# Kernel tuning notes

Hardware: AMD Instinct MI355X
Metric: run time of the kernel (lower is better)

The kernel has to match this reference:

```python
import jax, jax.numpy as jnp
import numpy as np

N_NODES = 65536
N_EDGES = 1048576
IN_FEATS = 128
N_HIDDEN = 64
N_LAYERS = 2
EPS = 1e-12  # matches torch F.normalize default eps


def setup_inputs() -> dict:
    key = jax.random.key(0)
    ks = jax.random.split(key, 8)
    features = jax.random.normal(ks[0], (N_NODES, IN_FEATS), dtype=jnp.float32)
    src = jax.random.randint(ks[1], (N_EDGES,), 0, N_NODES)
    dst = jax.random.randint(ks[2], (N_EDGES,), 0, N_NODES)
    W1 = jax.random.normal(ks[3], (IN_FEATS, N_HIDDEN), dtype=jnp.float32) * (1.0 / np.sqrt(IN_FEATS))
    b1 = jax.random.normal(ks[4], (N_HIDDEN,), dtype=jnp.float32) * 0.01
    W2 = jax.random.normal(ks[5], (N_HIDDEN, N_HIDDEN), dtype=jnp.float32) * (1.0 / np.sqrt(N_HIDDEN))
    b2 = jax.random.normal(ks[6], (N_HIDDEN,), dtype=jnp.float32) * 0.01
    betas = jnp.ones((N_LAYERS,), dtype=jnp.float32)  # init_beta=1, learnable
    return {"features": features, "src": src, "dst": dst,
            "W1": W1, "b1": b1, "W2": W2, "b2": b2, "betas": betas}


def agnn_conv(h, src, dst, beta, n_nodes):
    # L2-normalize node features (F.normalize, p=2)
    norm = jnp.sqrt(jnp.sum(h * h, axis=-1, keepdims=True))
    nh = h / jnp.maximum(norm, EPS)
    # cosine similarity along each edge: e_ij = beta * <nh_src, nh_dst>
    cos = jnp.sum(nh[src] * nh[dst], axis=-1)          # [E]
    e = beta * cos
    # edge softmax over incoming edges of each dst node (numerically stable)
    m = jax.ops.segment_max(e, dst, num_segments=n_nodes)   # [N], -inf for 0-in-degree
    ex = jnp.exp(e - m[dst])                                 # [E]
    s = jax.ops.segment_sum(ex, dst, num_segments=n_nodes)   # [N]
    alpha = ex / s[dst]                                      # [E]
    # weighted aggregation of UN-normalized source features
    out = jax.ops.segment_sum(alpha[:, None] * h[src], dst, num_segments=n_nodes)
    return out


def reference(features, src, dst, W1, b1, W2, b2, betas):
    h = jax.nn.relu(features @ W1 + b1)        # proj: Linear + ReLU
    for i in range(N_LAYERS):                   # stacked AGNNConv layers
        h = agnn_conv(h, src, dst, betas[i], N_NODES)
    return h @ W2 + b2                          # cls: Linear
```

## Files before the change

### kernel.cpp

```cpp
#include <hip/hip_runtime.h>

#define N_NODES 65536
#define N_EDGES 1048576
#define IN_FEATS 128
#define N_HIDDEN 64

static constexpr float F_EPS = 1e-12f;

template <int K, bool RELU, bool RN>
__device__ __forceinline__ void gemm_body(const float* __restrict__ A,
                                          const float* __restrict__ W,
                                          const float* __restrict__ bias,
                                          float* __restrict__ C,
                                          float* __restrict__ rn,
                                          int block64, int tid, float* Wl) {
  int lane = tid & 63;
  int wave = tid >> 6;
  float bv = bias[lane];
  int r0 = block64 * 64 + wave * 16;

  float a[16][K / 64];
#pragma unroll
  for (int r = 0; r < 16; ++r)
#pragma unroll
    for (int c = 0; c < K / 64; ++c)
      a[r][c] = A[(size_t)(r0 + r) * K + c * 64 + lane];

  float acc[16];
#pragma unroll
  for (int r = 0; r < 16; ++r) acc[r] = bv;

  const float4* W4 = reinterpret_cast<const float4*>(W);
  float4* Wl4 = reinterpret_cast<float4*>(Wl);

#pragma unroll
  for (int c = 0; c < K / 64; ++c) {
    __syncthreads();
#pragma unroll
    for (int i = tid; i < 64 * 16; i += 256) Wl4[i] = W4[c * 64 * 16 + i];
    __syncthreads();
#pragma unroll 8
    for (int kk = 0; kk < 64; ++kk) {
      float w = Wl[kk * 64 + lane];
#pragma unroll
      for (int r = 0; r < 16; ++r) {
        float av = __uint_as_float(
            __builtin_amdgcn_readlane(__float_as_uint(a[r][c]), kk));
        acc[r] = fmaf(av, w, acc[r]);
      }
    }
  }

#pragma unroll
  for (int r = 0; r < 16; ++r) {
    float v = acc[r];
    if (RELU) v = fmaxf(v, 0.0f);
    C[(size_t)(r0 + r) * 64 + lane] = v;
    if (RN) {
      float ss = v * v;
#pragma unroll
      for (int off = 32; off > 0; off >>= 1) ss += __shfl_xor(ss, off, 64);
      if (lane == 0) rn[r0 + r] = 1.0f / fmaxf(sqrtf(ss), F_EPS);
    }
  }
}

__global__ __launch_bounds__(256) void proj_scatter_k(
    const float* __restrict__ A, const float* __restrict__ W,
    const float* __restrict__ bias, float* __restrict__ C, float* __restrict__ rn,
    const int* __restrict__ src, const int* __restrict__ dst,
    int* __restrict__ deg2, int* __restrict__ csr) {
  __shared__ float Wl[64 * 64];
  int bb = blockIdx.x;
  int g = bb / 5;
  int r = bb % 5;
  if (r == 4) {
    gemm_body<IN_FEATS, true, true>(A, W, bias, C, rn, g, threadIdx.x, Wl);
  } else {
    int t = (g * 4 + r) * 256 + threadIdx.x;
    int d = dst[t];
    int s = src[t];
    int rep = t & 1;
    int p = atomicAdd(&deg2[rep * N_NODES + d], 1);
    if (p < 32) csr[(d << 6) + (rep << 5) + p] = s;
  }
}

template <int K, bool RELU, bool RN>
__global__ __launch_bounds__(256) void gemm64_k(const float* __restrict__ A,
                                                const float* __restrict__ W,
                                                const float* __restrict__ bias,
                                                float* __restrict__ C,
                                                float* __restrict__ rn) {
  __shared__ float Wl[64 * 64];
  gemm_body<K, RELU, RN>(A, W, bias, C, rn, blockIdx.x, threadIdx.x, Wl);
}

__global__ __launch_bounds__(256) void agnn_k(const float* __restrict__ X,
                                              const float* __restrict__ rn,
                                              const int* __restrict__ deg2,
                                              const int* __restrict__ csr,
                                              const float* __restrict__ betas, int layer,
                                              float* __restrict__ Y,
                                              float* __restrict__ rn_out) {
  int node = blockIdx.x * 4 + (threadIdx.x >> 6);
  int lane = threadIdx.x & 63;
  int sl = lane & 3;
  int g = lane >> 2;
  float beta = betas[layer];

  const float4* X4 = reinterpret_cast<const float4*>(X);
  float4 hd[4];
#pragma unroll
  for (int q = 0; q < 4; ++q) hd[q] = X4[(size_t)node * 16 + sl + 4 * q];
  float rnd = rn[node] * beta;

  int d0 = deg2[node];
  int d1 = deg2[N_NODES + node];
  d0 = d0 > 32 ? 32 : d0;
  d1 = d1 > 32 ? 32 : d1;
  int d = d0 + d1;
  int base = node << 6;

  float ssum = 0.0f;
  float4 acc[4];
#pragma unroll
  for (int q = 0; q < 4; ++q) acc[q] = make_float4(0.f, 0.f, 0.f, 0.f);

  bool act0 = (g < d);
  int slot0 = (g < d0) ? g : (g - d0 + 32);
  int s0 = act0 ? csr[base + slot0] : node;
  float4 hs0[4];
#pragma unroll
  for (int q = 0; q < 4; ++q) hs0[q] = X4[(size_t)s0 * 16 + sl + 4 * q];
  float rs0 = rn[s0];

  for (int i = 0; i < d; i += 16) {
    int j1 = i + 16 + g;
    bool act1 = (j1 < d);
    int slot1 = (j1 < d0) ? j1 : (j1 - d0 + 32);
    int s1 = act1 ? csr[base + slot1] : node;
    float4 hs1[4];
#pragma unroll
    for (int q = 0; q < 4; ++q) hs1[q] = X4[(size_t)s1 * 16 + sl + 4 * q];
    float rs1 = rn[s1];

    float pa = hd[0].x * hs0[0].x;
    pa = fmaf(hd[0].y, hs0[0].y, pa);
    pa = fmaf(hd[0].z, hs0[0].z, pa);
    pa = fmaf(hd[0].w, hs0[0].w, pa);
    pa = fmaf(hd[1].x, hs0[1].x, pa);
    pa = fmaf(hd[1].y, hs0[1].y, pa);
    pa = fmaf(hd[1].z, hs0[1].z, pa);
    pa = fmaf(hd[1].w, hs0[1].w, pa);
    float pb = hd[2].x * hs0[2].x;
    pb = fmaf(hd[2].y, hs0[2].y, pb);
    pb = fmaf(hd[2].z, hs0[2].z, pb);
    pb = fmaf(hd[2].w, hs0[2].w, pb);
    pb = fmaf(hd[3].x, hs0[3].x, pb);
    pb = fmaf(hd[3].y, hs0[3].y, pb);
    pb = fmaf(hd[3].z, hs0[3].z, pb);
    pb = fmaf(hd[3].w, hs0[3].w, pb);
    float p = pa + pb;
    p += __shfl_xor(p, 1, 64);
    p += __shfl_xor(p, 2, 64);
    float ex = act0 ? __expf(p * rnd * rs0) : 0.0f;
    ssum += ex;
#pragma unroll
    for (int q = 0; q < 4; ++q) {
      acc[q].x = fmaf(ex, hs0[q].x, acc[q].x);
      acc[q].y = fmaf(ex, hs0[q].y, acc[q].y);
      acc[q].z = fmaf(ex, hs0[q].z, acc[q].z);
      acc[q].w = fmaf(ex, hs0[q].w, acc[q].w);
    }

#pragma unroll
    for (int q = 0; q < 4; ++q) hs0[q] = hs1[q];
    rs0 = rs1;
    act0 = act1;
  }

#pragma unroll
  for (int off = 4; off < 64; off <<= 1) {
    ssum += __shfl_xor(ssum, off, 64);
#pragma unroll
    for (int q = 0; q < 4; ++q) {
      acc[q].x += __shfl_xor(acc[q].x, off, 64);
      acc[q].y += __shfl_xor(acc[q].y, off, 64);
      acc[q].z += __shfl_xor(acc[q].z, off, 64);
      acc[q].w += __shfl_xor(acc[q].w, off, 64);
    }
  }

  float inv = (ssum > 0.0f) ? (1.0f / ssum) : 0.0f;
#pragma unroll
  for (int q = 0; q < 4; ++q) {
    acc[q].x *= inv; acc[q].y *= inv; acc[q].z *= inv; acc[q].w *= inv;
  }

  if (g == 0) {
    float4* Y4 = reinterpret_cast<float4*>(Y);
#pragma unroll
    for (int q = 0; q < 4; ++q) Y4[(size_t)node * 16 + sl + 4 * q] = acc[q];
  }

  float ss = 0.0f;
#pragma unroll
  for (int q = 0; q < 4; ++q)
    ss += acc[q].x * acc[q].x + acc[q].y * acc[q].y +
          acc[q].z * acc[q].z + acc[q].w * acc[q].w;
  ss += __shfl_xor(ss, 1, 64);
  ss += __shfl_xor(ss, 2, 64);
  if (lane == 0) rn_out[node] = 1.0f / fmaxf(sqrtf(ss), F_EPS);
}

extern "C" void kernel_launch(void* const* d_in, const int* in_sizes, int n_in,
                              void* d_out, int out_size, void* d_ws, size_t ws_size,
                              hipStream_t stream) {
  const float* features = (const float*)d_in[0];
  const int* src = (const int*)d_in[1];
  const int* dst = (const int*)d_in[2];
  const float* W1 = (const float*)d_in[3];
  const float* b1 = (const float*)d_in[4];
  const float* W2 = (const float*)d_in[5];
  const float* b2 = (const float*)d_in[6];
  const float* betas = (const float*)d_in[7];
  float* out = (float*)d_out;

  char* ws = (char*)d_ws;
  size_t off = 0;
  auto alloc = [&](size_t bytes) {
    void* p = ws + off;
    off += (bytes + 255) & ~255UL;
    return p;
  };
  float* hA = (float*)alloc((size_t)N_NODES * 64 * 4);
  float* hB = (float*)alloc((size_t)N_NODES * 64 * 4);
  float* rnA = (float*)alloc((size_t)N_NODES * 4);
  float* rnB = (float*)alloc((size_t)N_NODES * 4);
  int* deg2 = (int*)alloc((size_t)2 * N_NODES * 4);
  int* csr = (int*)alloc((size_t)N_NODES * 64 * 4);

  hipMemsetAsync(deg2, 0, (size_t)2 * N_NODES * 4, stream);

  proj_scatter_k<<<5120, 256, 0, stream>>>(features, W1, b1, hA, rnA,
                                           src, dst, deg2, csr);

  agnn_k<<<N_NODES / 4, 256, 0, stream>>>(hA, rnA, deg2, csr, betas, 0, hB, rnB);

  agnn_k<<<N_NODES / 4, 256, 0, stream>>>(hB, rnB, deg2, csr, betas, 1, hA, rnA);

  gemm64_k<N_HIDDEN, false, false><<<N_NODES / 64, 256, 0, stream>>>(hA, W2, b2, out, nullptr);
}
```

Before: 312.0 us.

## Build CSR via two-pass bucketed scatter with shared-memory atomics

Replaces the single global-atomic scatter into a split two-replica CSR with a two-pass build. The first pass buckets edges by destination range in shared memory and flushes them in chunks to global buckets. The second pass, fused with the projection GEMM, places each bucket's edges into a contiguous per-node CSR using shared-memory atomics. This removes heavy global atomic contention and the replica slot arithmetic in the aggregation kernel, at the cost of an extra kernel launch and an intermediate buffer round trip. Fixed bucket capacities (BCAP, and a per-node cap of 64) can silently drop edges on skewed inputs.

Measured after the change: 391.2 us. 25.4% more time.

```diff
diff --git a/kernel.cpp b/kernel.cpp
--- a/kernel.cpp
+++ b/kernel.cpp
@@ -4,8 +4,51 @@
 #define N_EDGES 1048576
 #define IN_FEATS 128
 #define N_HIDDEN 64
+#define NBUCK 128
+#define BCAP 10240
+#define LCAP 40
 
 static constexpr float F_EPS = 1e-12f;
+
+__global__ __launch_bounds__(256) void passA_bucket_k(const int* __restrict__ src,
+                                                      const int* __restrict__ dst,
+                                                      int* __restrict__ gcnt,
+                                                      int2* __restrict__ gbuf) {
+  __shared__ int lcnt[NBUCK];
+  __shared__ int2 lbuf[NBUCK][LCAP];
+  int tid = threadIdx.x;
+  int b = blockIdx.x;
+  if (tid < NBUCK) lcnt[tid] = 0;
+  __syncthreads();
+
+  for (int i = b * 4096 + tid; i < (b + 1) * 4096; i += 256) {
+    int d = dst[i];
+    int s = src[i];
+    int k = d >> 9;
+    int p = atomicAdd(&lcnt[k], 1);
+    if (p < LCAP) {
+      lbuf[k][p] = make_int2(s, d);
+    } else {
+      int gp = atomicAdd(&gcnt[k], 1);
+      gbuf[(size_t)k * BCAP + gp] = make_int2(s, d);
+    }
+  }
+  __syncthreads();
+
+  int lane = tid & 63;
+  int w = tid >> 6;
+  for (int kk = 0; kk < 32; ++kk) {
+    int k = w * 32 + kk;
+    int L = lcnt[k];
+    L = L < LCAP ? L : LCAP;
+    if (L == 0) continue;
+    int pos;
+    if (lane == 0) pos = atomicAdd(&gcnt[k], L);
+    pos = __shfl(pos, 0, 64);
+    for (int j = lane; j < L; j += 64)
+      gbuf[(size_t)k * BCAP + pos + j] = lbuf[k][j];
+  }
+}
 
 template <int K, bool RELU, bool RN>
 __device__ __forceinline__ void gemm_body(const float* __restrict__ A,
@@ -65,24 +108,35 @@
   }
 }
 
-__global__ __launch_bounds__(256) void proj_scatter_k(
+__global__ __launch_bounds__(256) void place_proj_k(
     const float* __restrict__ A, const float* __restrict__ W,
     const float* __restrict__ bias, float* __restrict__ C, float* __restrict__ rn,
-    const int* __restrict__ src, const int* __restrict__ dst,
-    int* __restrict__ deg2, int* __restrict__ csr) {
+    const int* __restrict__ gcnt, const int2* __restrict__ gbuf,
+    int* __restrict__ deg, int* __restrict__ csr) {
   __shared__ float Wl[64 * 64];
   int bb = blockIdx.x;
-  int g = bb / 5;
-  int r = bb % 5;
-  if (r == 4) {
-    gemm_body<IN_FEATS, true, true>(A, W, bias, C, rn, g, threadIdx.x, Wl);
+  int g = bb / 9;
+  int r = bb % 9;
+  if (r == 8) {
+    int tid = threadIdx.x;
+    int* lcnt = (int*)Wl;
+    for (int j = tid; j < 512; j += 256) lcnt[j] = 0;
+    __syncthreads();
+    int E = gcnt[g];
+    E = E < BCAP ? E : BCAP;
+    for (int i = tid; i < E; i += 256) {
+      int2 e = gbuf[(size_t)g * BCAP + i];
+      int nn = e.y & 511;
+      int rk = atomicAdd(&lcnt[nn], 1);
+      if (rk < 64) csr[((size_t)e.y << 6) + rk] = e.x;
+    }
+    __syncthreads();
+    for (int j = tid; j < 512; j += 256) {
+      int dv = lcnt[j];
+      deg[g * 512 + j] = dv < 64 ? dv : 64;
+    }
   } else {
-    int t = (g * 4 + r) * 256 + threadIdx.x;
-    int d = dst[t];
-    int s = src[t];
-    int rep = t & 1;
-    int p = atomicAdd(&deg2[rep * N_NODES + d], 1);
-    if (p < 32) csr[(d << 6) + (rep << 5) + p] = s;
+    gemm_body<IN_FEATS, true, true>(A, W, bias, C, rn, g * 8 + r, threadIdx.x, Wl);
   }
 }
 
@@ -98,7 +152,7 @@
 
 __global__ __launch_bounds__(256) void agnn_k(const float* __restrict__ X,
                                               const float* __restrict__ rn,
-                                              const int* __restrict__ deg2,
+                                              const int* __restrict__ deg,
                                               const int* __restrict__ csr,
                                               const float* __restrict__ betas, int layer,
                                               float* __restrict__ Y,
@@ -115,11 +169,7 @@
   for (int q = 0; q < 4; ++q) hd[q] = X4[(size_t)node * 16 + sl + 4 * q];
   float rnd = rn[node] * beta;
 
-  int d0 = deg2[node];
-  int d1 = deg2[N_NODES + node];
-  d0 = d0 > 32 ? 32 : d0;
-  d1 = d1 > 32 ? 32 : d1;
-  int d = d0 + d1;
+  int d = deg[node];
   int base = node << 6;
 
   float ssum = 0.0f;
@@ -128,8 +178,7 @@
   for (int q = 0; q < 4; ++q) acc[q] = make_float4(0.f, 0.f, 0.f, 0.f);
 
   bool act0 = (g < d);
-  int slot0 = (g < d0) ? g : (g - d0 + 32);
-  int s0 = act0 ? csr[base + slot0] : node;
+  int s0 = act0 ? csr[base + g] : node;
   float4 hs0[4];
 #pragma unroll
   for (int q = 0; q < 4; ++q) hs0[q] = X4[(size_t)s0 * 16 + sl + 4 * q];
@@ -138,8 +187,7 @@
   for (int i = 0; i < d; i += 16) {
     int j1 = i + 16 + g;
     bool act1 = (j1 < d);
-    int slot1 = (j1 < d0) ? j1 : (j1 - d0 + 32);
-    int s1 = act1 ? csr[base + slot1] : node;
+    int s1 = act1 ? csr[base + j1] : node;
     float4 hs1[4];
 #pragma unroll
     for (int q = 0; q < 4; ++q) hs1[q] = X4[(size_t)s1 * 16 + sl + 4 * q];
@@ -238,17 +286,19 @@
   float* hB = (float*)alloc((size_t)N_NODES * 64 * 4);
   float* rnA = (float*)alloc((size_t)N_NODES * 4);
   float* rnB = (float*)alloc((size_t)N_NODES * 4);
-  int* deg2 = (int*)alloc((size_t)2 * N_NODES * 4);
+  int* deg = (int*)alloc((size_t)N_NODES * 4);
   int* csr = (int*)alloc((size_t)N_NODES * 64 * 4);
-
-  hipMemsetAsync(deg2, 0, (size_t)2 * N_NODES * 4, stream);
-
-  proj_scatter_k<<<5120, 256, 0, stream>>>(features, W1, b1, hA, rnA,
-                                           src, dst, deg2, csr);
-
-  agnn_k<<<N_NODES / 4, 256, 0, stream>>>(hA, rnA, deg2, csr, betas, 0, hB, rnB);
-
-  agnn_k<<<N_NODES / 4, 256, 0, stream>>>(hB, rnB, deg2, csr, betas, 1, hA, rnA);
+  int2* gbuf = (int2*)alloc((size_t)NBUCK * BCAP * 8);
+  int* gcnt = (int*)alloc((size_t)NBUCK * 4);
+
+  hipMemsetAsync(gcnt, 0, (size_t)NBUCK * 4, stream);
+  passA_bucket_k<<<256, 256, 0, stream>>>(src, dst, gcnt, gbuf);
+  place_proj_k<<<1152, 256, 0, stream>>>(features, W1, b1, hA, rnA,
+                                         gcnt, gbuf, deg, csr);
+
+  agnn_k<<<N_NODES / 4, 256, 0, stream>>>(hA, rnA, deg, csr, betas, 0, hB, rnB);
+
+  agnn_k<<<N_NODES / 4, 256, 0, stream>>>(hB, rnB, deg, csr, betas, 1, hA, rnA);
 
   gemm64_k<N_HIDDEN, false, false><<<N_NODES / 64, 256, 0, stream>>>(hA, W2, b2, out, nullptr);
 }
```
